# Performance work log

Measured on AMD Instinct MI355X. Metric: run time of the kernel, lower is better.

## Reference

```python
import jax, jax.numpy as jnp
import numpy as np

N_HEADS = 16


def setup_inputs() -> dict:
    key = jax.random.key(0)
    k_x, k_q, k_k, k_v, k_o = jax.random.split(key, 5)
    N, S, D = 8, 4096, 1024
    scale = 0.02
    return {
        "x": jax.random.normal(k_x, (N, S, D), dtype=jnp.float32),
        "Wq": jax.random.normal(k_q, (D, D), dtype=jnp.float32) * scale,
        "Wk": jax.random.normal(k_k, (D, D), dtype=jnp.float32) * scale,
        "Wv": jax.random.normal(k_v, (D, D), dtype=jnp.float32) * scale,
        "Wo": jax.random.normal(k_o, (D, D), dtype=jnp.float32) * scale,
        "bo": jnp.zeros((D,), dtype=jnp.float32),
    }


def reference(x, Wq, Wk, Wv, Wo, bo):
    N, S, D = x.shape
    H = N_HEADS
    hd = D // H
    # torch nn.Linear: y = x @ W.T (no bias for q/k/v)
    q = (x @ Wq.T).reshape(N, S, H, hd).transpose(0, 2, 1, 3)  # (N, H, S, hd)
    k = (x @ Wk.T).reshape(N, S, H, hd).transpose(0, 2, 1, 3)
    v = (x @ Wv.T).reshape(N, S, H, hd).transpose(0, 2, 1, 3)
    # Faithful to source: labels q/k bind to the HEADS axis of the permuted
    # tensors, h binds to the sequence axis -> attention over heads, shape
    # (N, S, H, H).
    att = jnp.einsum('nqhd,nkhd->nhqk', q, k)
    att = jax.nn.softmax(att / jnp.sqrt(jnp.asarray(hd, x.dtype)), axis=3)
    out = jnp.einsum('nhqk,nkhd->nqhd', att, v).reshape(N, S, D)
    return out @ Wo.T + bo
```

## Files before the change

kernel.cpp:

```cpp
#include <hip/hip_runtime.h>
#include <hip/hip_bf16.h>
#include <stdint.h>

typedef __hip_bfloat16 bf16;
typedef __attribute__((ext_vector_type(8))) short short8;
typedef __attribute__((ext_vector_type(4))) float f32x4;

__device__ __forceinline__ unsigned short f2bf(float f) {
    bf16 h = __float2bfloat16(f);
    union { bf16 h; unsigned short u; } c; c.h = h; return c.u;
}
__device__ __forceinline__ unsigned int pack2(float a, float b) {
    return (unsigned int)f2bf(a) | ((unsigned int)f2bf(b) << 16);
}

__device__ __forceinline__ void gld16(const void* g, void* l) {
    __builtin_amdgcn_global_load_lds(
        (const __attribute__((address_space(1))) void*)g,
        (__attribute__((address_space(3))) void*)l, 16, 0, 0);
}

__global__ __launch_bounds__(256) void cvt_f32_bf16(
    const float* __restrict__ in, unsigned short* __restrict__ out, long n4)
{
    long i = (long)blockIdx.x * 256 + threadIdx.x;
    if (i >= n4) return;
    float4 v = ((const float4*)in)[i];
    ushort4 o;
    o.x = f2bf(v.x); o.y = f2bf(v.y); o.z = f2bf(v.z); o.w = f2bf(v.w);
    ((ushort4*)out)[i] = o;
}

__global__ __launch_bounds__(256) void cvt_w4(
    const float* __restrict__ a, const float* __restrict__ b,
    const float* __restrict__ c, const float* __restrict__ d,
    unsigned short* __restrict__ out)
{
    const float* src = (blockIdx.y == 0) ? a : (blockIdx.y == 1) ? b
                     : (blockIdx.y == 2) ? c : d;
    long i = (long)blockIdx.x * 256 + threadIdx.x;
    float4 v = ((const float4*)src)[i];
    ushort4 o;
    o.x = f2bf(v.x); o.y = f2bf(v.y); o.z = f2bf(v.z); o.w = f2bf(v.w);
    ((ushort4*)(out + (size_t)blockIdx.y * 1048576))[i] = o;
}


__device__ __forceinline__ void store_c(bf16* C, size_t idx, float v) {
    C[idx] = __float2bfloat16(v);
}
__device__ __forceinline__ void store_c(float* C, size_t idx, float v) {
    C[idx] = v;
}

template <typename CT>
__device__ __forceinline__ void gemm_body256(
    const bf16* __restrict__ A, const bf16* __restrict__ B,
    CT* __restrict__ C, const float* __restrict__ bias,
    int M, int N, int K)
{
    __shared__ char smem[131072];

    const int t    = threadIdx.x;
    const int lane = t & 63;
    const int wave = t >> 6;
    const int wm   = wave >> 2;
    const int wn   = wave & 3;
    const int l16  = lane & 15;
    const int quad = lane >> 4;

    const int gy   = M >> 8;
    const int nwg  = (N >> 8) * gy;
    const int orig = blockIdx.x;
    const int wg   = (orig & 7) * (nwg >> 3) + (orig >> 3);
    const int bx   = wg / gy;
    const int by   = wg - bx * gy;

    const int rowBase = by << 8;
    const int colBase = bx << 8;

    size_t offA[4], offB[4];
    int ldsOff[4];
#pragma unroll
    for (int r = 0; r < 4; ++r) {
        int i   = (r << 9) + t;
        int row = i >> 3;
        int sw  = ((i & 7) << 4) ^ ((row & 7) << 4);
        offA[r] = (size_t)(rowBase + row) * K + (sw >> 1);
        offB[r] = (size_t)(colBase + row) * K + (sw >> 1);
        ldsOff[r] = i << 4;
    }

    auto stage = [&](int bufsel, int k0) {
        char* bA_ = smem + (bufsel << 16);
        char* bB_ = bA_ + 32768;
#pragma unroll
        for (int r = 0; r < 4; ++r) {
            gld16(A + offA[r] + k0, bA_ + ldsOff[r]);
            gld16(B + offB[r] + k0, bB_ + ldsOff[r]);
        }
    };

    f32x4 acc[8][4];
#pragma unroll
    for (int i = 0; i < 8; ++i)
#pragma unroll
        for (int j = 0; j < 4; ++j) acc[i][j] = (f32x4){0.f, 0.f, 0.f, 0.f};

    const int xr   = (l16 & 7) << 4;
    const int kq0  = ((quad << 4)) ^ xr;
    const int kq1  = (64 + (quad << 4)) ^ xr;
    const int aRowB = ((wm << 7) + l16) << 7;
    const int bRowB = ((wn << 6) + l16) << 7;

    stage(0, 0);
    stage(1, 64);
    asm volatile("s_waitcnt vmcnt(8)" ::: "memory");
    __builtin_amdgcn_s_barrier();

    const int ntiles = K >> 6;
    int cur = 0;
    for (int tt = 0; tt < ntiles; ++tt) {
        char* sA = smem + (cur << 16);
        char* sB = sA + 32768;

        short8 a0[8], b0[4];
#pragma unroll
        for (int mt = 0; mt < 8; ++mt)
            a0[mt] = *(const short8*)(sA + aRowB + mt * 2048 + kq0);
#pragma unroll
        for (int nt2 = 0; nt2 < 4; ++nt2)
            b0[nt2] = *(const short8*)(sB + bRowB + nt2 * 2048 + kq0);

        __builtin_amdgcn_s_setprio(1);
#pragma unroll
        for (int mt = 0; mt < 8; ++mt)
#pragma unroll
            for (int nt2 = 0; nt2 < 4; ++nt2)
                acc[mt][nt2] = __builtin_amdgcn_mfma_f32_16x16x32_bf16(
                    a0[mt], b0[nt2], acc[mt][nt2], 0, 0, 0);
        __builtin_amdgcn_s_setprio(0);

        short8 a1[8], b1[4];
#pragma unroll
        for (int mt = 0; mt < 8; ++mt)
            a1[mt] = *(const short8*)(sA + aRowB + mt * 2048 + kq1);
#pragma unroll
        for (int nt2 = 0; nt2 < 4; ++nt2)
            b1[nt2] = *(const short8*)(sB + bRowB + nt2 * 2048 + kq1);

        asm volatile("s_waitcnt lgkmcnt(0)" ::: "memory");
        __builtin_amdgcn_s_barrier();

        if (tt + 2 < ntiles) stage(cur, (tt + 2) << 6);

        __builtin_amdgcn_s_setprio(1);
#pragma unroll
        for (int mt = 0; mt < 8; ++mt)
#pragma unroll
            for (int nt2 = 0; nt2 < 4; ++nt2)
                acc[mt][nt2] = __builtin_amdgcn_mfma_f32_16x16x32_bf16(
                    a1[mt], b1[nt2], acc[mt][nt2], 0, 0, 0);
        __builtin_amdgcn_s_setprio(0);

        if (tt + 1 < ntiles) {
            if (tt + 2 < ntiles)
                asm volatile("s_waitcnt vmcnt(8)" ::: "memory");
            else
                asm volatile("s_waitcnt vmcnt(0)" ::: "memory");
            __builtin_amdgcn_s_barrier();
        }
        cur ^= 1;
    }

#pragma unroll
    for (int nt2 = 0; nt2 < 4; ++nt2) {
        int col = colBase + (wn << 6) + (nt2 << 4) + l16;
        float bv = bias ? bias[col] : 0.f;
#pragma unroll
        for (int mt = 0; mt < 8; ++mt) {
            int row0 = rowBase + (wm << 7) + (mt << 4) + (quad << 2);
#pragma unroll
            for (int r = 0; r < 4; ++r)
                store_c(C, (size_t)(row0 + r) * N + col, acc[mt][nt2][r] + bv);
        }
    }
}

__global__ __launch_bounds__(512, 2) void gemm_qkv(
    const bf16* __restrict__ A, const bf16* __restrict__ B,
    bf16* __restrict__ C, int M, int N, int K)
{
    gemm_body256<bf16>(A, B, C, nullptr, M, N, K);
}

__global__ __launch_bounds__(512, 2) void gemm_proj(
    const bf16* __restrict__ A, const bf16* __restrict__ B,
    float* __restrict__ C, const float* __restrict__ bias,
    int M, int N, int K)
{
    gemm_body256<float>(A, B, C, bias, M, N, K);
}

__global__ __launch_bounds__(256) void attn_heads(
    const bf16* __restrict__ QKV, bf16* __restrict__ Y)
{
    __shared__ char smem[4 * 3264];
    const int t    = threadIdx.x;
    const int lane = t & 63;
    const int wave = t >> 6;
    const int l16  = lane & 15;
    const int quad = lane >> 4;

    char* Vp = smem + wave * 3264;
    char* Pp = smem + wave * 3264 + 2240;

    const long pos = (long)blockIdx.x * 4 + wave;
    const int  n   = (int)(pos >> 12);
    const int  s   = (int)(pos & 4095);
    const bf16* base = QKV + pos * 3072;

    uint4 v0 = *(const uint4*)(base + 2048 + lane * 8);
    uint4 v1 = *(const uint4*)(base + 2560 + lane * 8);
    short8 qa0 = *(const short8*)(base +        l16 * 64 + quad * 8);
    short8 qa1 = *(const short8*)(base +        l16 * 64 + quad * 8 + 32);
    short8 kb0 = *(const short8*)(base + 1024 + l16 * 64 + quad * 8);
    short8 kb1 = *(const short8*)(base + 1024 + l16 * 64 + quad * 8 + 32);

    {
        int kh0 = lane >> 3, c = lane & 7;
        *(uint4*)(Vp + kh0 * 136 + c * 16) = v0;
        *(uint4*)(Vp + (kh0 + 8) * 136 + c * 16) = v1;
    }

    *(f32x4*)(Pp + lane * 16) = (f32x4){0.f, 0.f, 0.f, 0.f};

    f32x4 sacc = (f32x4){0.f, 0.f, 0.f, 0.f};
    sacc = __builtin_amdgcn_mfma_f32_16x16x32_bf16(qa0, kb0, sacc, 0, 0, 0);
    sacc = __builtin_amdgcn_mfma_f32_16x16x32_bf16(qa1, kb1, sacc, 0, 0, 0);

    float e[4], sm[4];
#pragma unroll
    for (int r = 0; r < 4; r++) { e[r] = __expf(sacc[r] * 0.125f); sm[r] = e[r]; }
#pragma unroll
    for (int m = 1; m <= 8; m <<= 1) {
#pragma unroll
        for (int r = 0; r < 4; r++) sm[r] += __shfl_xor(sm[r], m);
    }
#pragma unroll
    for (int r = 0; r < 4; r++) {
        float p = e[r] * __builtin_amdgcn_rcpf(sm[r]);
        *(unsigned short*)(Pp + (quad * 4 + r) * 64 + l16 * 2) = f2bf(p);
    }

    short8 pfrag = *(const short8*)(Pp + l16 * 64 + quad * 16);

    const char* gbase = Vp + (quad & 1) * (8 * 136)
                           + ((l16 >> 3) * 16) + ((l16 & 7) * 2);
    const size_t yb = ((size_t)n * 4096 + (size_t)(s >> 4)) * 1024
                    + (size_t)(s & 15) * 64;
#pragma unroll
    for (int f = 0; f < 4; f++) {
        short8 vfrag;
#pragma unroll
        for (int j = 0; j < 8; j++)
            vfrag[j] = *(const short*)(gbase + f * 32 + j * 136);
        f32x4 oc = __builtin_amdgcn_mfma_f32_16x16x32_bf16(
            vfrag, pfrag, (f32x4){0.f, 0.f, 0.f, 0.f}, 0, 0, 0);
        uint2 w;
        w.x = pack2(oc[0], oc[1]);
        w.y = pack2(oc[2], oc[3]);
        *(uint2*)(Y + yb + (size_t)l16 * 262144 + 16 * f + quad * 4) = w;
    }
}

extern "C" void kernel_launch(void* const* d_in, const int* in_sizes, int n_in,
                              void* d_out, int out_size, void* d_ws, size_t ws_size,
                              hipStream_t stream) {
    const float* x  = (const float*)d_in[0];
    const float* Wq = (const float*)d_in[1];
    const float* Wk = (const float*)d_in[2];
    const float* Wv = (const float*)d_in[3];
    const float* Wo = (const float*)d_in[4];
    const float* bo = (const float*)d_in[5];
    float* out = (float*)d_out;

    const int M = 8 * 4096;
    const size_t MN = (size_t)M * 1024;

    bf16* Qkv  = (bf16*)d_ws;
    bf16* Xb   = Qkv + (size_t)M * 3072;
    bf16* Yb   = Xb;
    bf16* Wcat = Xb + MN;
    bf16* Wob  = Wcat + (size_t)3072 * 1024;

    {
        long n4 = (long)MN / 4;
        cvt_f32_bf16<<<dim3((unsigned)(n4 / 256)), dim3(256), 0, stream>>>(
            x, (unsigned short*)Xb, n4);
        cvt_w4<<<dim3(1024, 4), dim3(256), 0, stream>>>(
            Wq, Wk, Wv, Wo, (unsigned short*)Wcat);
    }

    dim3 block(512);
    gemm_qkv<<<dim3((3072 / 256) * (M / 256)), block, 0, stream>>>(
        Xb, Wcat, Qkv, M, 3072, 1024);
    attn_heads<<<dim3(M / 4), dim3(256), 0, stream>>>(Qkv, Yb);
    gemm_proj<<<dim3((1024 / 256) * (M / 256)), block, 0, stream>>>(
        Yb, Wob, out, bo, M, 1024, 1024);
}
```

Before: 592.4 us.

## Software-pipeline LDS fragment reads with MFMA clusters in GEMM main loop

Splits each K-tile's MFMA work into four 4x4 clusters and interleaves LDS fragment reads for the next cluster with the current one, prefetching the next tile's first fragments across the barrier. Staging of the tile two ahead is moved to after the first barrier, and 64-bit offsets become 32-bit ints with a shared LDS base to cut address registers. The goal is to hide LDS latency behind MFMA issue. The cost is more live fragment registers, and 32-bit offsets could overflow for larger matrices.

```diff
diff --git a/kernel.cpp b/kernel.cpp
--- a/kernel.cpp
+++ b/kernel.cpp
@@ -79,25 +79,24 @@
     const int rowBase = by << 8;
     const int colBase = bx << 8;
 
-    size_t offA[4], offB[4];
-    int ldsOff[4];
+    int offA[4], offB[4];
 #pragma unroll
     for (int r = 0; r < 4; ++r) {
         int i   = (r << 9) + t;
         int row = i >> 3;
         int sw  = ((i & 7) << 4) ^ ((row & 7) << 4);
-        offA[r] = (size_t)(rowBase + row) * K + (sw >> 1);
-        offB[r] = (size_t)(colBase + row) * K + (sw >> 1);
-        ldsOff[r] = i << 4;
-    }
+        offA[r] = (rowBase + row) * K + (sw >> 1);
+        offB[r] = (colBase + row) * K + (sw >> 1);
+    }
+    const int ldsBase = t << 4;
 
     auto stage = [&](int bufsel, int k0) {
         char* bA_ = smem + (bufsel << 16);
         char* bB_ = bA_ + 32768;
 #pragma unroll
         for (int r = 0; r < 4; ++r) {
-            gld16(A + offA[r] + k0, bA_ + ldsOff[r]);
-            gld16(B + offB[r] + k0, bB_ + ldsOff[r]);
+            gld16(A + offA[r] + k0, bA_ + ldsBase + (r << 13));
+            gld16(B + offB[r] + k0, bB_ + ldsBase + (r << 13));
         }
     };
 
@@ -107,16 +106,42 @@
 #pragma unroll
         for (int j = 0; j < 4; ++j) acc[i][j] = (f32x4){0.f, 0.f, 0.f, 0.f};
 
-    const int xr   = (l16 & 7) << 4;
-    const int kq0  = ((quad << 4)) ^ xr;
-    const int kq1  = (64 + (quad << 4)) ^ xr;
+    const int xr    = (l16 & 7) << 4;
+    const int kq0   = ((quad << 4)) ^ xr;
+    const int kq1   = (64 + (quad << 4)) ^ xr;
     const int aRowB = ((wm << 7) + l16) << 7;
     const int bRowB = ((wn << 6) + l16) << 7;
+
+    auto rdA = [&](short8* dst, char* sA, int mtbase, int kq) {
+#pragma unroll
+        for (int m = 0; m < 4; ++m)
+            dst[m] = *(const short8*)(sA + aRowB + (mtbase + m) * 2048 + kq);
+    };
+    auto rdB = [&](short8* dst, char* sB, int kq) {
+#pragma unroll
+        for (int n = 0; n < 4; ++n)
+            dst[n] = *(const short8*)(sB + bRowB + n * 2048 + kq);
+    };
+    auto cluster = [&](const short8* af, const short8* bfr, int mtbase) {
+        __builtin_amdgcn_sched_barrier(0);
+        __builtin_amdgcn_s_setprio(1);
+#pragma unroll
+        for (int m = 0; m < 4; ++m)
+#pragma unroll
+            for (int n = 0; n < 4; ++n)
+                acc[mtbase + m][n] = __builtin_amdgcn_mfma_f32_16x16x32_bf16(
+                    af[m], bfr[n], acc[mtbase + m][n], 0, 0, 0);
+        __builtin_amdgcn_s_setprio(0);
+    };
 
     stage(0, 0);
     stage(1, 64);
     asm volatile("s_waitcnt vmcnt(8)" ::: "memory");
     __builtin_amdgcn_s_barrier();
+
+    short8 A0[4], A1[4], B0[4], B1[4];
+    rdA(A0, smem, 0, kq0);
+    rdB(B0, smem + 32768, kq0);
 
     const int ntiles = K >> 6;
     int cur = 0;
@@ -124,52 +149,30 @@
         char* sA = smem + (cur << 16);
         char* sB = sA + 32768;
 
-        short8 a0[8], b0[4];
-#pragma unroll
-        for (int mt = 0; mt < 8; ++mt)
-            a0[mt] = *(const short8*)(sA + aRowB + mt * 2048 + kq0);
-#pragma unroll
-        for (int nt2 = 0; nt2 < 4; ++nt2)
-            b0[nt2] = *(const short8*)(sB + bRowB + nt2 * 2048 + kq0);
-
-        __builtin_amdgcn_s_setprio(1);
-#pragma unroll
-        for (int mt = 0; mt < 8; ++mt)
-#pragma unroll
-            for (int nt2 = 0; nt2 < 4; ++nt2)
-                acc[mt][nt2] = __builtin_amdgcn_mfma_f32_16x16x32_bf16(
-                    a0[mt], b0[nt2], acc[mt][nt2], 0, 0, 0);
-        __builtin_amdgcn_s_setprio(0);
-
-        short8 a1[8], b1[4];
-#pragma unroll
-        for (int mt = 0; mt < 8; ++mt)
-            a1[mt] = *(const short8*)(sA + aRowB + mt * 2048 + kq1);
-#pragma unroll
-        for (int nt2 = 0; nt2 < 4; ++nt2)
-            b1[nt2] = *(const short8*)(sB + bRowB + nt2 * 2048 + kq1);
+        rdA(A1, sA, 4, kq0);
+        cluster(A0, B0, 0);
+        rdA(A0, sA, 0, kq1);
+        rdB(B1, sB, kq1);
+        cluster(A1, B0, 4);
+        rdA(A1, sA, 4, kq1);
+        cluster(A0, B1, 0);
 
         asm volatile("s_waitcnt lgkmcnt(0)" ::: "memory");
-        __builtin_amdgcn_s_barrier();
-
-        if (tt + 2 < ntiles) stage(cur, (tt + 2) << 6);
-
-        __builtin_amdgcn_s_setprio(1);
-#pragma unroll
-        for (int mt = 0; mt < 8; ++mt)
-#pragma unroll
-            for (int nt2 = 0; nt2 < 4; ++nt2)
-                acc[mt][nt2] = __builtin_amdgcn_mfma_f32_16x16x32_bf16(
-                    a1[mt], b1[nt2], acc[mt][nt2], 0, 0, 0);
-        __builtin_amdgcn_s_setprio(0);
-
+        __builtin_amdgcn_sched_barrier(0);
         if (tt + 1 < ntiles) {
-            if (tt + 2 < ntiles)
+            __builtin_amdgcn_s_barrier();
+            if (tt + 2 < ntiles) {
+                stage(cur, (tt + 2) << 6);
                 asm volatile("s_waitcnt vmcnt(8)" ::: "memory");
-            else
+            } else {
                 asm volatile("s_waitcnt vmcnt(0)" ::: "memory");
+            }
             __builtin_amdgcn_s_barrier();
+            char* nA = smem + ((cur ^ 1) << 16);
+            rdA(A0, nA, 0, kq0);
+            rdB(B0, nA + 32768, kq0);
         }
+        cluster(A1, B1, 4);
         cur ^= 1;
     }
 
```

After: 591.8 us. No clear change (-0.1%).
